# Kernel tuning notes

Hardware: AMD Instinct MI355X
Metric: run time of the kernel (lower is better)

The kernel has to match this reference:

```python
import jax, jax.numpy as jnp
import numpy as np

EMBED = 1024
HEADS = 16
HEAD_DIM = EMBED // HEADS
B, S = 4, 2048


def setup_inputs() -> dict:
    key = jax.random.key(0)
    ks = jax.random.split(key, 12)
    scale = 1.0 / np.sqrt(EMBED)
    inp = {
        'query': jax.random.normal(ks[0], (B, S, EMBED), jnp.float32),
        'key_in': jax.random.normal(ks[1], (B, S, EMBED), jnp.float32),
        'value': jax.random.normal(ks[2], (B, S, EMBED), jnp.float32),
        'mask': jnp.tril(jnp.ones((S, S), jnp.int32))[None, None],  # causal [1,1,S,S]
        'Wq': jax.random.normal(ks[3], (EMBED, EMBED), jnp.float32) * scale,
        'bq': jnp.zeros((EMBED,), jnp.float32),
        'Wk': jax.random.normal(ks[4], (EMBED, EMBED), jnp.float32) * scale,
        'bk': jnp.zeros((EMBED,), jnp.float32),
        'Wv': jax.random.normal(ks[5], (EMBED, EMBED), jnp.float32) * scale,
        'bv': jnp.zeros((EMBED,), jnp.float32),
        'Wo': jax.random.normal(ks[6], (EMBED, EMBED), jnp.float32) * scale,
        'bo': jnp.zeros((EMBED,), jnp.float32),
    }
    return inp


def reference(query, key_in, value, mask, Wq, bq, Wk, bk, Wv, bv, Wo, bo):
    b = query.shape[0]
    # projections (torch Linear: x @ W.T + b)
    Q = query @ Wq.T + bq
    K = key_in @ Wk.T + bk
    V = value @ Wv.T + bv
    # [B, H, S, Dh]
    Q = Q.reshape(b, -1, HEADS, HEAD_DIM).transpose(0, 2, 1, 3)
    K = K.reshape(b, -1, HEADS, HEAD_DIM).transpose(0, 2, 1, 3)
    V = V.reshape(b, -1, HEADS, HEAD_DIM).transpose(0, 2, 1, 3)
    scores = jnp.einsum('bhqd,bhkd->bhqk', Q, K) / np.sqrt(HEAD_DIM)
    scores = jnp.where(mask == 0, jnp.float32(-1e20), scores)
    probs = jax.nn.softmax(scores, axis=-1)  # dropout p=0 (eval)
    attn = jnp.einsum('bhqk,bhkd->bhqd', probs, V)
    attn = attn.transpose(0, 2, 1, 3).reshape(b, -1, EMBED)
    return attn @ Wo.T + bo
```

## Files before the change

### kernel.cpp

```cpp
#include <hip/hip_runtime.h>
#include <type_traits>

typedef unsigned short u16;
typedef __bf16 bf16x8 __attribute__((ext_vector_type(8)));
typedef float f32x4 __attribute__((ext_vector_type(4)));

#define EMBED   1024
#define HEADS   16
#define HEAD_DIM 64
#define BATCH   4
#define SEQ     2048
#define MROWS   (BATCH * SEQ)

__device__ __forceinline__ u16 f2bf(float f) {
  union { __bf16 h; u16 u; } c;
  c.h = (__bf16)f;
  return c.u;
}

__device__ __forceinline__ bf16x8 cvt8(const float* p) {
  const float4 a = *(const float4*)p;
  const float4 b = *(const float4*)(p + 4);
  bf16x8 r;
  r[0] = (__bf16)a.x; r[1] = (__bf16)a.y; r[2] = (__bf16)a.z; r[3] = (__bf16)a.w;
  r[4] = (__bf16)b.x; r[5] = (__bf16)b.y; r[6] = (__bf16)b.z; r[7] = (__bf16)b.w;
  return r;
}

__device__ __forceinline__ void gload16(const u16* g, u16* lds) {
  __builtin_amdgcn_global_load_lds(
      (const __attribute__((address_space(1))) void*)g,
      (__attribute__((address_space(3))) void*)lds, 16, 0, 0);
}

__global__ __launch_bounds__(256) void cvt_bf16(
    const float* __restrict__ src, u16* __restrict__ dst, int n8)
{
  const int i = blockIdx.x * 256 + threadIdx.x;
  if (i < n8) *(bf16x8*)(dst + (size_t)i * 8) = cvt8(src + (size_t)i * 8);
}

__global__ __launch_bounds__(256) void cvt_fused(
    const float* q,  u16* dq,
    const float* k,  u16* dk,
    const float* wq, u16* dwq,
    const float* wk, u16* dwk,
    const float* wv, u16* dwv,
    const float* wo, u16* dwo,
    int n8t, int n8w)
{
  int i = blockIdx.x * 256 + threadIdx.x;
  if (i < n8t) { *(bf16x8*)(dq + (size_t)i * 8) = cvt8(q + (size_t)i * 8); return; }
  i -= n8t;
  if (i < n8t) { *(bf16x8*)(dk + (size_t)i * 8) = cvt8(k + (size_t)i * 8); return; }
  i -= n8t;
  if (i < n8w) { *(bf16x8*)(dwq + (size_t)i * 8) = cvt8(wq + (size_t)i * 8); return; }
  i -= n8w;
  if (i < n8w) { *(bf16x8*)(dwk + (size_t)i * 8) = cvt8(wk + (size_t)i * 8); return; }
  i -= n8w;
  if (i < n8w) { *(bf16x8*)(dwv + (size_t)i * 8) = cvt8(wv + (size_t)i * 8); return; }
  i -= n8w;
  if (dwo && i < n8w) { *(bf16x8*)(dwo + (size_t)i * 8) = cvt8(wo + (size_t)i * 8); }
}

template<typename TB, typename TC>
__global__ __launch_bounds__(256) void gemm_bt(
    const u16* __restrict__ A, const TB* __restrict__ Bw,
    const float* __restrict__ bias, TC* __restrict__ C,
    int M, int N, int K)
{
  __shared__ __align__(16) u16 As[128][32];
  __shared__ __align__(16) u16 Bs[128][32];
  const int t    = threadIdx.x;
  const int lane = t & 63;
  const int wave = t >> 6;
  const int quad = lane >> 4;
  const int lr   = lane & 15;
  const int m0 = blockIdx.y * 128;
  const int n0 = blockIdx.x * 128;
  const int wr = (wave >> 1) * 64;
  const int wc = (wave & 1) * 64;
  const int gr = lane >> 2;
  const int gc = (lane & 3) * 8;

  f32x4 acc[4][4] = {};

  for (int k0 = 0; k0 < K; k0 += 32) {
    gload16(&A[(size_t)(m0 + 16 * wave + gr) * K + k0 + gc],      &As[16 * wave][0]);
    gload16(&A[(size_t)(m0 + 64 + 16 * wave + gr) * K + k0 + gc], &As[64 + 16 * wave][0]);
    if constexpr (std::is_same<TB, u16>::value) {
      gload16(&Bw[(size_t)(n0 + 16 * wave + gr) * K + k0 + gc],      &Bs[16 * wave][0]);
      gload16(&Bw[(size_t)(n0 + 64 + 16 * wave + gr) * K + k0 + gc], &Bs[64 + 16 * wave][0]);
    } else {
      const int srr = t >> 2, src = (t & 3) * 8;
      *(bf16x8*)&Bs[srr][src]      = cvt8(&Bw[(size_t)(n0 + srr) * K + k0 + src]);
      *(bf16x8*)&Bs[64 + srr][src] = cvt8(&Bw[(size_t)(n0 + 64 + srr) * K + k0 + src]);
    }
    __syncthreads();
    bf16x8 af[4], bfr[4];
#pragma unroll
    for (int i = 0; i < 4; ++i) af[i]  = *(const bf16x8*)&As[wr + i * 16 + lr][quad * 8];
#pragma unroll
    for (int i = 0; i < 4; ++i) bfr[i] = *(const bf16x8*)&Bs[wc + i * 16 + lr][quad * 8];
#pragma unroll
    for (int mi = 0; mi < 4; ++mi)
#pragma unroll
      for (int ni = 0; ni < 4; ++ni)
        acc[mi][ni] = __builtin_amdgcn_mfma_f32_16x16x32_bf16(af[mi], bfr[ni], acc[mi][ni], 0, 0, 0);
    __syncthreads();
  }

#pragma unroll
  for (int mi = 0; mi < 4; ++mi)
#pragma unroll
    for (int ni = 0; ni < 4; ++ni) {
      const int col = n0 + wc + ni * 16 + lr;
      const float bv = bias[col];
#pragma unroll
      for (int r = 0; r < 4; ++r) {
        const int row = m0 + wr + mi * 16 + quad * 4 + r;
        const float v = acc[mi][ni][r] + bv;
        if constexpr (std::is_same<TC, u16>::value)
          C[(size_t)row * N + col] = f2bf(v);
        else
          C[(size_t)row * N + col] = v;
      }
    }
}

__global__ __launch_bounds__(256) void gemm_vt(
    const u16* __restrict__ A, const u16* __restrict__ Bw,
    const float* __restrict__ bias, u16* __restrict__ Vt,
    int M, int N, int K)
{
  __shared__ __align__(16) u16 As[128][32];
  __shared__ __align__(16) u16 Bs[128][32];
  const int t    = threadIdx.x;
  const int lane = t & 63;
  const int wave = t >> 6;
  const int quad = lane >> 4;
  const int lr   = lane & 15;
  const int m0 = blockIdx.y * 128;
  const int n0 = blockIdx.x * 128;
  const int wr = (wave >> 1) * 64;
  const int wc = (wave & 1) * 64;
  const int gr = lane >> 2;
  const int gc = (lane & 3) * 8;

  f32x4 acc[4][4] = {};

  for (int k0 = 0; k0 < K; k0 += 32) {
    gload16(&A[(size_t)(m0 + 16 * wave + gr) * K + k0 + gc],       &As[16 * wave][0]);
    gload16(&A[(size_t)(m0 + 64 + 16 * wave + gr) * K + k0 + gc],  &As[64 + 16 * wave][0]);
    gload16(&Bw[(size_t)(n0 + 16 * wave + gr) * K + k0 + gc],      &Bs[16 * wave][0]);
    gload16(&Bw[(size_t)(n0 + 64 + 16 * wave + gr) * K + k0 + gc], &Bs[64 + 16 * wave][0]);
    __syncthreads();
    bf16x8 af[4], bfr[4];
#pragma unroll
    for (int i = 0; i < 4; ++i) af[i]  = *(const bf16x8*)&As[wr + i * 16 + lr][quad * 8];
#pragma unroll
    for (int i = 0; i < 4; ++i) bfr[i] = *(const bf16x8*)&Bs[wc + i * 16 + lr][quad * 8];
#pragma unroll
    for (int mi = 0; mi < 4; ++mi)
#pragma unroll
      for (int ni = 0; ni < 4; ++ni)
        acc[mi][ni] = __builtin_amdgcn_mfma_f32_16x16x32_bf16(af[mi], bfr[ni], acc[mi][ni], 0, 0, 0);
    __syncthreads();
  }

#pragma unroll
  for (int mi = 0; mi < 4; ++mi)
#pragma unroll
    for (int ni = 0; ni < 4; ++ni) {
      const int col = n0 + wc + ni * 16 + lr;
      const int hh = col >> 6, dd = col & 63;
      const float bv = bias[col];
      const int row0 = m0 + wr + mi * 16 + quad * 4;
      const int bb = row0 >> 11, s0 = row0 & 2047;
      u16 pk[4];
#pragma unroll
      for (int r = 0; r < 4; ++r) pk[r] = f2bf(acc[mi][ni][r] + bv);
      *(ushort4*)&Vt[((size_t)((bb * 16 + hh) * 64 + dd)) * SEQ + s0] = *(ushort4*)pk;
    }
}

#define QS_OFF 0
#define PS_OFF (64 * 72)
#define KV_OFF (2 * 64 * 72)
#define TILE_SZ (64 * 64)
__global__ __launch_bounds__(256, 3) void flash5(
    const u16* __restrict__ Qbf, const u16* __restrict__ Wqb,
    const float* __restrict__ bq,
    const u16* __restrict__ Kp, const u16* __restrict__ Vt,
    u16* __restrict__ AO)
{
  __shared__ __align__(16) u16 smem[KV_OFF + 4 * TILE_SZ];
  u16 (*Qs)[72] = (u16(*)[72])(smem + QS_OFF);
  u16 (*Ps)[72] = (u16(*)[72])(smem + PS_OFF);

  const int t    = threadIdx.x;
  const int lane = t & 63;
  const int wave = t >> 6;
  const int quad = lane >> 4;
  const int lr   = lane & 15;
  const int bh = blockIdx.x;
  const int pr = blockIdx.y;
  const int b  = bh >> 4, h = bh & 15;
  const size_t rowbase = (size_t)b * SEQ;
  const int hcol = h * HEAD_DIM;
  const int wrow = wave * 16;
  const int sr = lane >> 3;
  const int sc = ((lane & 7) ^ sr) * 8;

  auto frag = [&](int off, int row, int chunk) -> bf16x8 {
    return *(const bf16x8*)(smem + off + row * 64 + ((chunk ^ (row & 7)) << 3));
  };

  int q0 = 0;

  auto stageQW = [&](int bi, int k0) {
    const int ko = KV_OFF + bi * TILE_SZ;
    const int vo = KV_OFF + (2 + bi) * TILE_SZ;
#pragma unroll
    for (int c8 = 0; c8 < 2; ++c8) {
      const int g = wrow + c8 * 8;
      gload16(&Qbf[(rowbase + q0 + g + sr) * EMBED + k0 + sc], smem + ko + g * 64);
      gload16(&Wqb[(size_t)(hcol + g + sr) * EMBED + k0 + sc], smem + vo + g * 64);
    }
  };
  auto stageKV = [&](int bi, int j) {
    const int kb = j * 64;
    const int ko = KV_OFF + bi * TILE_SZ;
    const int vo = KV_OFF + (2 + bi) * TILE_SZ;
#pragma unroll
    for (int c8 = 0; c8 < 2; ++c8) {
      const int g = wrow + c8 * 8;
      gload16(&Kp[(rowbase + kb + g + sr) * EMBED + hcol + sc], smem + ko + g * 64);
      gload16(&Vt[((size_t)bh * 64 + g + sr) * SEQ + kb + sc],  smem + vo + g * 64);
    }
  };

  for (int half = 0; half < 2; ++half) {
    const int qi = half ? (31 - pr) : pr;
    q0 = qi * 64;

    f32x4 qacc[4] = {};
    stageQW(0, 0);
    __syncthreads();
    for (int s = 0; s < 16; ++s) {
      if (s < 15) stageQW((s + 1) & 1, (s + 1) * 64);
      const int ao = KV_OFF + (s & 1) * TILE_SZ;
      const int bo = KV_OFF + (2 + (s & 1)) * TILE_SZ;
#pragma unroll
      for (int ks = 0; ks < 2; ++ks) {
        const bf16x8 aq = frag(ao, wrow + lr, ks * 4 + quad);
        bf16x8 bw[4];
#pragma unroll
        for (int ni = 0; ni < 4; ++ni) bw[ni] = frag(bo, ni * 16 + lr, ks * 4 + quad);
#pragma unroll
        for (int ni = 0; ni < 4; ++ni)
          qacc[ni] = __builtin_amdgcn_mfma_f32_16x16x32_bf16(aq, bw[ni], qacc[ni], 0, 0, 0);
      }
      __syncthreads();
    }
#pragma unroll
    for (int ni = 0; ni < 4; ++ni) {
      const float bv = bq[hcol + ni * 16 + lr];
#pragma unroll
      for (int r = 0; r < 4; ++r)
        Qs[wrow + quad * 4 + r][ni * 16 + lr] = f2bf(qacc[ni][r] + bv);
    }

    f32x4 o_acc[4] = {};
    float lsum[4] = {0.f, 0.f, 0.f, 0.f};

    stageKV(0, 0);
    __syncthreads();
    for (int j = 0; j <= qi; ++j) {
      if (j < qi) stageKV((j + 1) & 1, j + 1);
      const int ko = KV_OFF + (j & 1) * TILE_SZ;
      const int vo = KV_OFF + (2 + (j & 1)) * TILE_SZ;

      f32x4 s[4] = {};
#pragma unroll
      for (int ks = 0; ks < 2; ++ks) {
        const bf16x8 a = *(const bf16x8*)&Qs[wrow + lr][ks * 32 + quad * 8];
        bf16x8 bk[4];
#pragma unroll
        for (int ni = 0; ni < 4; ++ni) bk[ni] = frag(ko, ni * 16 + lr, ks * 4 + quad);
#pragma unroll
        for (int ni = 0; ni < 4; ++ni)
          s[ni] = __builtin_amdgcn_mfma_f32_16x16x32_bf16(a, bk[ni], s[ni], 0, 0, 0);
      }
      const bool diag = (j == qi);
#pragma unroll
      for (int ni = 0; ni < 4; ++ni)
#pragma unroll
        for (int r = 0; r < 4; ++r) {
          float p = __expf(s[ni][r] * 0.125f);
          if (diag && (ni * 16 + lr > wrow + quad * 4 + r)) p = 0.f;
          lsum[r] += p;
          Ps[wrow + quad * 4 + r][ni * 16 + lr] = f2bf(p);
        }
#pragma unroll
      for (int ks = 0; ks < 2; ++ks) {
        const bf16x8 ap = *(const bf16x8*)&Ps[wrow + lr][ks * 32 + quad * 8];
        bf16x8 bv[4];
#pragma unroll
        for (int nd = 0; nd < 4; ++nd) bv[nd] = frag(vo, nd * 16 + lr, ks * 4 + quad);
#pragma unroll
        for (int nd = 0; nd < 4; ++nd)
          o_acc[nd] = __builtin_amdgcn_mfma_f32_16x16x32_bf16(ap, bv[nd], o_acc[nd], 0, 0, 0);
      }
      __syncthreads();
    }

    float linv[4];
#pragma unroll
    for (int r = 0; r < 4; ++r) {
      float l = lsum[r];
      for (int d = 1; d < 16; d <<= 1) l += __shfl_xor(l, d);
      linv[r] = 1.0f / l;
    }
#pragma unroll
    for (int nd = 0; nd < 4; ++nd)
#pragma unroll
      for (int r = 0; r < 4; ++r)
        AO[(rowbase + q0 + wrow + quad * 4 + r) * EMBED + hcol + nd * 16 + lr]
            = f2bf(o_acc[nd][r] * linv[r]);
  }
}

extern "C" void kernel_launch(void* const* d_in, const int* in_sizes, int n_in,
                              void* d_out, int out_size, void* d_ws, size_t ws_size,
                              hipStream_t stream) {
  const float* query  = (const float*)d_in[0];
  const float* key_in = (const float*)d_in[1];
  const float* value  = (const float*)d_in[2];
  const float* Wq = (const float*)d_in[4];
  const float* bq = (const float*)d_in[5];
  const float* Wk = (const float*)d_in[6];
  const float* bk = (const float*)d_in[7];
  const float* Wv = (const float*)d_in[8];
  const float* bv = (const float*)d_in[9];
  const float* Wo = (const float*)d_in[10];
  const float* bo = (const float*)d_in[11];
  float* out = (float*)d_out;

  const size_t tsz = (size_t)MROWS * EMBED;
  const size_t wsz = (size_t)EMBED * EMBED;

  u16* Kp = (u16*)d_ws;
  u16* Vt = Kp + tsz;
  const bool wo_bf = (ws_size >= (2 * tsz + wsz) * sizeof(u16));
  u16* Wob = wo_bf ? (Vt + tsz) : nullptr;

  u16* Qbf = (u16*)d_out;
  u16* Wqb = Qbf + tsz;
  u16* Wkb = Wqb + wsz;
  u16* Wvb = Wkb + wsz;

  u16* Kbf = (u16*)d_in[3];
  u16* Vbf = Kbf;
  u16* AO  = Kbf;

  dim3 blk(256);
  const int n8t = (int)(tsz / 8), n8w = (int)(wsz / 8);

  {
    const int total = 2 * n8t + (wo_bf ? 4 : 3) * n8w;
    cvt_fused<<<(total + 255) / 256, blk, 0, stream>>>(
        query, Qbf, key_in, Kbf, Wq, Wqb, Wk, Wkb, Wv, Wvb, Wo, Wob, n8t, n8w);
  }

  dim3 gproj(EMBED / 128, MROWS / 128);
  gemm_bt<u16, u16><<<gproj, blk, 0, stream>>>(Kbf, Wkb, bk, Kp, MROWS, EMBED, EMBED);

  cvt_bf16<<<n8t / 256, blk, 0, stream>>>(value, Vbf, n8t);
  gemm_vt<<<gproj, blk, 0, stream>>>(Vbf, Wvb, bv, Vt, MROWS, EMBED, EMBED);

  dim3 gattn(BATCH * HEADS, 16);
  flash5<<<gattn, blk, 0, stream>>>(Qbf, Wqb, bq, Kp, Vt, AO);

  if (wo_bf)
    gemm_bt<u16, float><<<gproj, blk, 0, stream>>>(AO, Wob, bo, out, MROWS, EMBED, EMBED);
  else
    gemm_bt<float, float><<<gproj, blk, 0, stream>>>(AO, Wo, bo, out, MROWS, EMBED, EMBED);
}
```

Baseline: 369.1 us.

## Swizzle GEMM block order, transpose attention MFMAs, add setprio, vectorize LDS stores

Remaps GEMM block indices into a grouped order so that blocks running at the same time share A and B tiles in L2. In the attention kernel, the MFMA operands for Q-projection and QK^T are swapped so each lane holds a full row's 4 consecutive columns. This allows packed 8-byte ushort4 stores into the Qs and Ps LDS tiles instead of scalar 2-byte stores, and reduces the row-sum reduction to two shuffles plus a broadcast. s_setprio is also raised around the MFMA bursts to favour matrix issue across waves. The swizzle hardcodes a grid width of 8, so any GEMM launched with a different grid x would compute wrong tile coordinates.

```diff
diff --git a/kernel.cpp b/kernel.cpp
--- a/kernel.cpp
+++ b/kernel.cpp
@@ -63,6 +63,15 @@
   if (dwo && i < n8w) { *(bf16x8*)(dwo + (size_t)i * 8) = cvt8(wo + (size_t)i * 8); }
 }
 
+__device__ __forceinline__ void swz_block(int& m0, int& n0) {
+  const int gx = 8;
+  int bid = blockIdx.y * gx + blockIdx.x;
+  const int cpx = (gx * 64) >> 3;
+  bid = (bid & 7) * cpx + (bid >> 3);
+  m0 = (bid / gx) * 128;
+  n0 = (bid - (bid / gx) * gx) * 128;
+}
+
 template<typename TB, typename TC>
 __global__ __launch_bounds__(256) void gemm_bt(
     const u16* __restrict__ A, const TB* __restrict__ Bw,
@@ -76,8 +85,8 @@
   const int wave = t >> 6;
   const int quad = lane >> 4;
   const int lr   = lane & 15;
-  const int m0 = blockIdx.y * 128;
-  const int n0 = blockIdx.x * 128;
+  int m0, n0;
+  swz_block(m0, n0);
   const int wr = (wave >> 1) * 64;
   const int wc = (wave & 1) * 64;
   const int gr = lane >> 2;
@@ -140,8 +149,8 @@
   const int wave = t >> 6;
   const int quad = lane >> 4;
   const int lr   = lane & 15;
-  const int m0 = blockIdx.y * 128;
-  const int n0 = blockIdx.x * 128;
+  int m0, n0;
+  swz_block(m0, n0);
   const int wr = (wave >> 1) * 64;
   const int wc = (wave & 1) * 64;
   const int gr = lane >> 2;
@@ -256,23 +265,28 @@
         const bf16x8 aq = frag(ao, wrow + lr, ks * 4 + quad);
         bf16x8 bw[4];
 #pragma unroll
-        for (int ni = 0; ni < 4; ++ni) bw[ni] = frag(bo, ni * 16 + lr, ks * 4 + quad);
-#pragma unroll
-        for (int ni = 0; ni < 4; ++ni)
-          qacc[ni] = __builtin_amdgcn_mfma_f32_16x16x32_bf16(aq, bw[ni], qacc[ni], 0, 0, 0);
+        for (int mi = 0; mi < 4; ++mi) bw[mi] = frag(bo, mi * 16 + lr, ks * 4 + quad);
+        __builtin_amdgcn_s_setprio(1);
+#pragma unroll
+        for (int mi = 0; mi < 4; ++mi)
+          qacc[mi] = __builtin_amdgcn_mfma_f32_16x16x32_bf16(bw[mi], aq, qacc[mi], 0, 0, 0);
+        __builtin_amdgcn_s_setprio(0);
       }
       __syncthreads();
     }
 #pragma unroll
-    for (int ni = 0; ni < 4; ++ni) {
-      const float bv = bq[hcol + ni * 16 + lr];
-#pragma unroll
-      for (int r = 0; r < 4; ++r)
-        Qs[wrow + quad * 4 + r][ni * 16 + lr] = f2bf(qacc[ni][r] + bv);
+    for (int mi = 0; mi < 4; ++mi) {
+      const float4 bv4 = *(const float4*)&bq[hcol + mi * 16 + quad * 4];
+      union { ushort4 v; u16 e[4]; } pk;
+      pk.e[0] = f2bf(qacc[mi][0] + bv4.x);
+      pk.e[1] = f2bf(qacc[mi][1] + bv4.y);
+      pk.e[2] = f2bf(qacc[mi][2] + bv4.z);
+      pk.e[3] = f2bf(qacc[mi][3] + bv4.w);
+      *(ushort4*)&Qs[wrow + lr][mi * 16 + quad * 4] = pk.v;
     }
 
     f32x4 o_acc[4] = {};
-    float lsum[4] = {0.f, 0.f, 0.f, 0.f};
+    float lsum = 0.f;
 
     stageKV(0, 0);
     __syncthreads();
@@ -281,47 +295,53 @@
       const int ko = KV_OFF + (j & 1) * TILE_SZ;
       const int vo = KV_OFF + (2 + (j & 1)) * TILE_SZ;
 
-      f32x4 s[4] = {};
+      f32x4 st[4] = {};
 #pragma unroll
       for (int ks = 0; ks < 2; ++ks) {
         const bf16x8 a = *(const bf16x8*)&Qs[wrow + lr][ks * 32 + quad * 8];
         bf16x8 bk[4];
 #pragma unroll
-        for (int ni = 0; ni < 4; ++ni) bk[ni] = frag(ko, ni * 16 + lr, ks * 4 + quad);
-#pragma unroll
-        for (int ni = 0; ni < 4; ++ni)
-          s[ni] = __builtin_amdgcn_mfma_f32_16x16x32_bf16(a, bk[ni], s[ni], 0, 0, 0);
+        for (int mi = 0; mi < 4; ++mi) bk[mi] = frag(ko, mi * 16 + lr, ks * 4 + quad);
+        __builtin_amdgcn_s_setprio(1);
+#pragma unroll
+        for (int mi = 0; mi < 4; ++mi)
+          st[mi] = __builtin_amdgcn_mfma_f32_16x16x32_bf16(bk[mi], a, st[mi], 0, 0, 0);
+        __builtin_amdgcn_s_setprio(0);
       }
       const bool diag = (j == qi);
 #pragma unroll
-      for (int ni = 0; ni < 4; ++ni)
+      for (int mi = 0; mi < 4; ++mi) {
+        union { ushort4 v; u16 e[4]; } pk;
 #pragma unroll
         for (int r = 0; r < 4; ++r) {
-          float p = __expf(s[ni][r] * 0.125f);
-          if (diag && (ni * 16 + lr > wrow + quad * 4 + r)) p = 0.f;
-          lsum[r] += p;
-          Ps[wrow + quad * 4 + r][ni * 16 + lr] = f2bf(p);
+          float p = __expf(st[mi][r] * 0.125f);
+          if (diag && (mi * 16 + quad * 4 + r > wrow + lr)) p = 0.f;
+          lsum += p;
+          pk.e[r] = f2bf(p);
         }
+        *(ushort4*)&Ps[wrow + lr][mi * 16 + quad * 4] = pk.v;
+      }
 #pragma unroll
       for (int ks = 0; ks < 2; ++ks) {
         const bf16x8 ap = *(const bf16x8*)&Ps[wrow + lr][ks * 32 + quad * 8];
         bf16x8 bv[4];
 #pragma unroll
         for (int nd = 0; nd < 4; ++nd) bv[nd] = frag(vo, nd * 16 + lr, ks * 4 + quad);
+        __builtin_amdgcn_s_setprio(1);
 #pragma unroll
         for (int nd = 0; nd < 4; ++nd)
           o_acc[nd] = __builtin_amdgcn_mfma_f32_16x16x32_bf16(ap, bv[nd], o_acc[nd], 0, 0, 0);
+        __builtin_amdgcn_s_setprio(0);
       }
       __syncthreads();
     }
 
+    lsum += __shfl_xor(lsum, 16);
+    lsum += __shfl_xor(lsum, 32);
     float linv[4];
 #pragma unroll
-    for (int r = 0; r < 4; ++r) {
-      float l = lsum[r];
-      for (int d = 1; d < 16; d <<= 1) l += __shfl_xor(l, d);
-      linv[r] = 1.0f / l;
-    }
+    for (int r = 0; r < 4; ++r)
+      linv[r] = 1.0f / __shfl(lsum, quad * 4 + r);
 #pragma unroll
     for (int nd = 0; nd < 4; ++nd)
 #pragma unroll
```

After: 365.9 us. No clear change (-0.9%).
